# Optimization experiments

Measured on AMD Instinct MI355X. Metric: run time of the kernel, lower is better.

## Reference

```python
import jax, jax.numpy as jnp
import numpy as np
import math

B, T, D, H = 8, 1024, 512, 8
DK = D // H


def setup_inputs() -> dict:
    key = jax.random.key(0)
    ks = jax.random.split(key, 16)
    f = lambda k, s: jax.random.normal(k, s, dtype=jnp.float32)
    p = lambda k, s: jax.random.normal(k, s, dtype=jnp.float32) * 0.02
    return {
        "query": f(ks[0], (B, T, D)),
        "key": f(ks[1], (B, T, D)),
        "value": f(ks[2], (B, T, D)),
        "pos_embedding": f(ks[3], (B, T, D)),
        "Wq": p(ks[4], (D, D)), "bq": p(ks[5], (D,)),
        "Wk": p(ks[6], (D, D)), "bk": p(ks[7], (D,)),
        "Wv": p(ks[8], (D, D)), "bv": p(ks[9], (D,)),
        "Wp": p(ks[10], (D, D)),
        "u_bias": p(ks[11], (H, DK)),
        "v_bias": p(ks[12], (H, DK)),
        "Wo": p(ks[13], (D, D)), "bo": p(ks[14], (D,)),
    }


def _rel_shift(pos_score):
    # pos_score: [B, H, T, T]  -> Transformer-XL relative shift via pad/reshape
    b, h, t1, t2 = pos_score.shape
    padded = jnp.concatenate(
        [jnp.zeros((b, h, t1, 1), pos_score.dtype), pos_score], axis=-1
    )  # [B,H,T,T+1]
    padded = padded.reshape(b, h, t2 + 1, t1)
    return padded[:, :, 1:].reshape(b, h, t1, t2)


def reference(query, key, value, pos_embedding, Wq, bq, Wk, bk, Wv, bv, Wp,
              u_bias, v_bias, Wo, bo):
    q = (query @ Wq + bq).reshape(B, T, H, DK)          # [B,T,H,DK]
    k = (key @ Wk + bk).reshape(B, T, H, DK)
    v = (value @ Wv + bv).reshape(B, T, H, DK)
    p = (pos_embedding @ Wp).reshape(B, T, H, DK)

    content_score = jnp.einsum("bihd,bjhd->bhij", q + u_bias, k)
    pos_score = jnp.einsum("bihd,bjhd->bhij", q + v_bias, p)
    pos_score = _rel_shift(pos_score)

    score = (content_score + pos_score) / math.sqrt(D)  # note: sqrt(d_model)
    attn = jax.nn.softmax(score, axis=-1)               # dropout: eval mode
    context = jnp.einsum("bhij,bjhd->bihd", attn, v).reshape(B, T, D)
    return context @ Wo + bo
```

## Files before the change

### kernel.cpp

```cpp
#include <hip/hip_runtime.h>

#define B_ 8
#define T_ 1024
#define D_ 512
#define H_ 8
#define DK_ 64

typedef __bf16 bf16x8 __attribute__((ext_vector_type(8)));
typedef float f32x4 __attribute__((ext_vector_type(4)));

#define MFMA16(a, b, c) __builtin_amdgcn_mfma_f32_16x16x32_bf16(a, b, c, 0, 0, 0)

__device__ __forceinline__ bf16x8 pack8(float4 a, float4 b) {
  bf16x8 r;
  r[0] = (__bf16)a.x; r[1] = (__bf16)a.y; r[2] = (__bf16)a.z; r[3] = (__bf16)a.w;
  r[4] = (__bf16)b.x; r[5] = (__bf16)b.y; r[6] = (__bf16)b.z; r[7] = (__bf16)b.w;
  return r;
}

__device__ __forceinline__ void load_lds16(const void* g, void* l) {
  __builtin_amdgcn_global_load_lds(
      (const __attribute__((address_space(1))) void*)g,
      (__attribute__((address_space(3))) void*)l, 16, 0, 0);
}

__global__ __launch_bounds__(256) void cvt_w(const float* __restrict__ w0,
                                             const float* __restrict__ w1,
                                             const float* __restrict__ w2,
                                             const float* __restrict__ w3,
                                             const float* __restrict__ w4,
                                             __bf16* __restrict__ wt) {
  __shared__ float Ts[64][65];
  const float* W = (blockIdx.z == 0) ? w0
                 : (blockIdx.z == 1) ? w1
                 : (blockIdx.z == 2) ? w2
                 : (blockIdx.z == 3) ? w3 : w4;
  const int tid = threadIdx.x;
  const int kt = blockIdx.x * 64, nt = blockIdx.y * 64;
  const int r = tid >> 2, co = (tid & 3) * 16;
#pragma unroll
  for (int q = 0; q < 4; ++q)
    *(float4*)&Ts[r][co + q * 4] =
        *(const float4*)(W + (size_t)(kt + r) * 512 + nt + co + q * 4);
  __syncthreads();
  bf16x8 o0, o1;
#pragma unroll
  for (int q = 0; q < 8; ++q) o0[q] = (__bf16)Ts[co + q][r];
#pragma unroll
  for (int q = 0; q < 8; ++q) o1[q] = (__bf16)Ts[co + 8 + q][r];
  const int key = r & 7;
  __bf16* dst =
      wt + (size_t)blockIdx.z * 262144 + (size_t)(nt + r) * 512 + kt;
  *(bf16x8*)(dst + (((co >> 3) ^ key) << 3)) = o0;
  *(bf16x8*)(dst + ((((co >> 3) + 1) ^ key) << 3)) = o1;
}

__global__ __launch_bounds__(256, 4) void gemm_dma(
    const float* __restrict__ qf, const float* __restrict__ kf,
    const float* __restrict__ vf, const float* __restrict__ pf,
    const __bf16* __restrict__ Wt, const float* __restrict__ bq,
    const float* __restrict__ bk, const float* __restrict__ bv,
    const float* __restrict__ ub, const float* __restrict__ vb,
    __bf16* __restrict__ quB, __bf16* __restrict__ qvB,
    __bf16* __restrict__ kB, __bf16* __restrict__ vT,
    __bf16* __restrict__ pB) {
  __shared__ __bf16 smem[17408];
  __bf16* As = smem;
  __bf16* Bs = smem + 8192;
  const int tid = threadIdx.x;
  const int z = blockIdx.z;
  const int wave = tid >> 6, lane = tid & 63, l16 = lane & 15, quad = lane >> 4;
  const int wm = wave & 1, wn = wave >> 1;
  const int m0 = blockIdx.x * 128, n0 = blockIdx.y * 128;

  const float* Af = (z == 0) ? qf : (z == 1) ? kf : (z == 2) ? vf : pf;
  const __bf16* Bg = Wt + (size_t)z * (512 * 512);

  const int drow = tid >> 3, dch = (tid & 7) * 8;
  char* ldsB = (char*)Bs + (tid & 192) * 16;
  const int keyc = l16 & 7;

  f32x4 acc[4][4];
#pragma unroll
  for (int rb = 0; rb < 4; ++rb)
#pragma unroll
    for (int cb = 0; cb < 4; ++cb) acc[rb][cb] = 0.f;

#pragma unroll 1
  for (int k0 = 0; k0 < 512; k0 += 64) {
    __syncthreads();
#pragma unroll
    for (int c4 = 0; c4 < 4; ++c4)
      load_lds16(Bg + (size_t)(n0 + c4 * 32 + drow) * 512 + k0 + dch,
                 ldsB + c4 * 4096);
#pragma unroll
    for (int c4 = 0; c4 < 4; ++c4) {
      const int row = c4 * 32 + drow;
      const float* s = Af + (size_t)(m0 + row) * 512 + k0 + dch;
      float4 a0 = *(const float4*)s;
      float4 a1 = *(const float4*)(s + 4);
      *(bf16x8*)&As[row * 64 + ((((dch >> 3) ^ row) & 7) << 3)] =
          pack8(a0, a1);
    }
    __syncthreads();
#pragma unroll
    for (int s = 0; s < 2; ++s) {
      const int ph = ((s * 4 + quad) ^ keyc) << 3;
      bf16x8 afr[4], bfr[4];
#pragma unroll
      for (int rb = 0; rb < 4; ++rb)
        afr[rb] = *(const bf16x8*)&As[(wm * 64 + rb * 16 + l16) * 64 + ph];
#pragma unroll
      for (int cb = 0; cb < 4; ++cb)
        bfr[cb] = *(const bf16x8*)&Bs[(wn * 64 + cb * 16 + l16) * 64 + ph];
#pragma unroll
      for (int rb = 0; rb < 4; ++rb)
#pragma unroll
        for (int cb = 0; cb < 4; ++cb)
          acc[rb][cb] = MFMA16(afr[rb], bfr[cb], acc[rb][cb]);
    }
  }

  __syncthreads();

  if (z == 2) {
    __bf16* Tt = smem;
#pragma unroll
    for (int rb = 0; rb < 4; ++rb)
#pragma unroll
      for (int cb = 0; cb < 4; ++cb) {
        const int cl = wn * 64 + cb * 16 + l16;
        const float bb = bv[n0 + cl];
#pragma unroll
        for (int r = 0; r < 4; ++r) {
          const int rl = wm * 64 + rb * 16 + quad * 4 + r;
          Tt[cl * 136 + rl] = (__bf16)(acc[rb][cb][r] + bb);
        }
      }
    __syncthreads();
    const int r2 = tid >> 1, ch = (tid & 1) * 64;
    const int hh = (n0 + r2) >> 6, dkk = (n0 + r2) & 63;
    const int bI = m0 >> 10, t0 = m0 & 1023;
    __bf16* dst = vT + (((size_t)(bI * H_ + hh)) * DK_ + dkk) * T_ + t0 + ch;
    const int vkey = dkk & 7;
#pragma unroll
    for (int q = 0; q < 8; ++q)
      *(bf16x8*)(dst + ((q ^ vkey) * 8)) =
          *(const bf16x8*)&Tt[r2 * 136 + ch + q * 8];
    return;
  }

  __bf16* Tt = smem;
  const int trow = tid & 127, hs = tid >> 7;
  const int bI = m0 >> 10, tt = (m0 & 1023) + trow;
  const int hh = (n0 >> 6) + hs;
  const size_t obase = (((size_t)(bI * H_ + hh)) * T_ + tt) * DK_;
  const int npass = (z == 0) ? 2 : 1;
#pragma unroll 1
  for (int pass = 0; pass < npass; ++pass) {
#pragma unroll
    for (int rb = 0; rb < 4; ++rb)
#pragma unroll
      for (int cb = 0; cb < 4; ++cb) {
        const int cl = wn * 64 + cb * 16 + l16;
        const int col = n0 + cl;
        const float b0 = (z == 0) ? bq[col] : (z == 1) ? bk[col] : 0.f;
        const float b1 = (z == 0) ? (pass ? vb[col] : ub[col]) : 0.f;
#pragma unroll
        for (int r = 0; r < 4; ++r) {
          const int rl = wm * 64 + rb * 16 + quad * 4 + r;
          Tt[rl * 136 + cl] = (__bf16)((acc[rb][cb][r] + b0) + b1);
        }
      }
    __syncthreads();
    __bf16* dst = ((z == 0) ? (pass ? qvB : quB) : (z == 1) ? kB : pB) + obase;
#pragma unroll
    for (int qd = 0; qd < 8; ++qd) {
      const int c = (z == 0) ? qd : (qd ^ (tt & 7));
      *(bf16x8*)(dst + c * 8) =
          *(const bf16x8*)&Tt[trow * 136 + hs * 64 + qd * 8];
    }
    if (pass + 1 < npass) __syncthreads();
  }
}

__global__ __launch_bounds__(256, 4) void gemm_out(
    const __bf16* __restrict__ ctxA, const __bf16* __restrict__ Wo,
    const float* __restrict__ bo, float* __restrict__ out) {
  __shared__ __bf16 As[4096];
  __shared__ __bf16 Bs[8192];
  const int tid = threadIdx.x;
  const int wave = tid >> 6, lane = tid & 63, l16 = lane & 15, quad = lane >> 4;
  const int m0 = blockIdx.x * 64, n0 = blockIdx.y * 128;

  const int drow = tid >> 3, dch = (tid & 7) * 8;
  char* ldsA = (char*)As + (tid & 192) * 16;
  char* ldsB = (char*)Bs + (tid & 192) * 16;
  const int keyc = l16 & 7;

  f32x4 acc[4][2];
#pragma unroll
  for (int rb = 0; rb < 4; ++rb)
#pragma unroll
    for (int cb = 0; cb < 2; ++cb) acc[rb][cb] = 0.f;

#pragma unroll 1
  for (int k0 = 0; k0 < 512; k0 += 64) {
    __syncthreads();
#pragma unroll
    for (int c4 = 0; c4 < 2; ++c4)
      load_lds16(ctxA + (size_t)(m0 + c4 * 32 + drow) * 512 + k0 + dch,
                 ldsA + c4 * 4096);
#pragma unroll
    for (int c4 = 0; c4 < 4; ++c4)
      load_lds16(Wo + (size_t)(n0 + c4 * 32 + drow) * 512 + k0 + dch,
                 ldsB + c4 * 4096);
    __syncthreads();
#pragma unroll
    for (int s = 0; s < 2; ++s) {
      const int ph = ((s * 4 + quad) ^ keyc) << 3;
      bf16x8 afr[4], bfr[2];
#pragma unroll
      for (int rb = 0; rb < 4; ++rb)
        afr[rb] = *(const bf16x8*)&As[(rb * 16 + l16) * 64 + ph];
#pragma unroll
      for (int cb = 0; cb < 2; ++cb)
        bfr[cb] = *(const bf16x8*)&Bs[(wave * 32 + cb * 16 + l16) * 64 + ph];
#pragma unroll
      for (int rb = 0; rb < 4; ++rb)
#pragma unroll
        for (int cb = 0; cb < 2; ++cb)
          acc[rb][cb] = MFMA16(afr[rb], bfr[cb], acc[rb][cb]);
    }
  }

#pragma unroll
  for (int rb = 0; rb < 4; ++rb)
#pragma unroll
    for (int cb = 0; cb < 2; ++cb) {
      const int col = n0 + wave * 32 + cb * 16 + l16;
      const float bb = bo[col];
#pragma unroll
      for (int r = 0; r < 4; ++r) {
        const int row = m0 + rb * 16 + quad * 4 + r;
        out[(size_t)row * 512 + col] = acc[rb][cb][r] + bb;
      }
    }
}

__global__ __launch_bounds__(256, 4) void attn_mfma(
    const __bf16* __restrict__ qu, const __bf16* __restrict__ qv,
    const __bf16* __restrict__ kbuf, const __bf16* __restrict__ vT,
    const __bf16* __restrict__ pbuf, __bf16* __restrict__ ctx) {
  constexpr float SCALE2 = 0.06375871865f;
  __shared__ __bf16 smemA[4488];
  __shared__ __bf16 Vt[4096];
  __shared__ __bf16 Pb[8192];
  __bf16* Kt = smemA;
  __bf16* Rs = smemA;
  __bf16* Pa = Pb;

  const int tid = threadIdx.x;
  const int wave = tid >> 6, lane = tid & 63, l16 = lane & 15, quad = lane >> 4;
  const int g = blockIdx.x;
  const int bhq = (g & 7) * 8 + (g >> 7);
  const int i0 = ((g >> 3) & 15) * 64;
  const size_t bh = (size_t)bhq * T_ * DK_;
  const __bf16* QU = qu + bh;
  const __bf16* QV = qv + bh;
  const __bf16* Kg = kbuf + bh;
  const __bf16* Vg = vT + bh;
  const __bf16* Pg = pbuf + bh;

  bf16x8 quA[2], qvw[2], qv4[2];
  {
    const int rw = i0 + wave * 16 + l16;
    const int r4g = i0 + 64 + l16;
    const int r4 = (r4g < T_) ? r4g : T_ - 1;
#pragma unroll
    for (int s = 0; s < 2; ++s) {
      const int ko = s * 32 + quad * 8;
      quA[s] = *(const bf16x8*)&QU[(size_t)rw * DK_ + ko];
      qvw[s] = *(const bf16x8*)&QV[(size_t)rw * DK_ + ko];
      qv4[s] = *(const bf16x8*)&QV[(size_t)r4 * DK_ + ko];
    }
  }

  f32x4 Oacc[4];
#pragma unroll
  for (int cb = 0; cb < 4; ++cb) Oacc[cb] = 0.f;
  float lrun[4];
#pragma unroll
  for (int r = 0; r < 4; ++r) lrun[r] = 0.f;

  const int rbase = wave * 16 + quad * 4;
  const int keyr = l16 & 7;
  const int keyp = (l16 + 7) & 7;
  const int drow = tid >> 3;
  const int dch = (tid & 7) * 8;
  char* ldsK = (char*)Kt + (tid & 192) * 16;
  char* ldsV = (char*)Vt + (tid & 192) * 16;
  char* ldsP = (char*)Pb + (tid & 192) * 16;

#pragma unroll 1
  for (int jt = 0; jt < 16; ++jt) {
    const int j0 = jt * 64;
    int cs = T_ - 65 + j0 - i0;
    if (cs < 0) cs += T_;
    if (cs >= T_) cs -= T_;

    __syncthreads();
    load_lds16(Kg + (size_t)(j0 + drow) * 64 + dch, ldsK);
    load_lds16(Kg + (size_t)(j0 + 32 + drow) * 64 + dch, ldsK + 4096);
    __builtin_amdgcn_sched_barrier(0);
    load_lds16(Vg + (size_t)drow * T_ + j0 + dch, ldsV);
    load_lds16(Vg + (size_t)(32 + drow) * T_ + j0 + dch, ldsV + 4096);
#pragma unroll
    for (int c = 0; c < 4; ++c) {
      int prow = cs + c * 32 + drow;
      if (prow >= T_) prow -= T_;
      load_lds16(Pg + (size_t)prow * 64 + dch, ldsP + c * 4096);
    }
    asm volatile("s_waitcnt vmcnt(6)" ::: "memory");
    __builtin_amdgcn_s_barrier();

    f32x4 sA[4];
#pragma unroll
    for (int cb = 0; cb < 4; ++cb) sA[cb] = 0.f;
    __builtin_amdgcn_s_setprio(1);
#pragma unroll
    for (int s = 0; s < 2; ++s)
#pragma unroll
      for (int cb = 0; cb < 4; ++cb) {
        bf16x8 kf = *(const bf16x8*)&Kt[(cb * 16 + l16) * 64 +
                                        (((s * 4 + quad) ^ keyr) << 3)];
        sA[cb] = MFMA16(quA[s], kf, sA[cb]);
      }
    __builtin_amdgcn_s_setprio(0);

    asm volatile("s_waitcnt vmcnt(0)" ::: "memory");
    __builtin_amdgcn_s_barrier();

    __builtin_amdgcn_s_setprio(1);
#pragma unroll
    for (int c = 0; c < 5; ++c) {
      const int cb = 3 - wave + c;
      f32x4 rc = 0.f;
#pragma unroll
      for (int s = 0; s < 2; ++s) {
        bf16x8 pf = *(const bf16x8*)&Pb[(cb * 16 + l16) * 64 +
                                        (((s * 4 + quad) ^ keyp) << 3)];
        rc = MFMA16(qvw[s], pf, rc);
      }
      const int col = cb * 16 + l16;
#pragma unroll
      for (int rr = 0; rr < 4; ++rr) {
        const int dj = col + rbase + rr - 64;
        if (dj >= 0 && dj < 64) Rs[(rbase + rr) * 68 + dj] = (__bf16)rc[rr];
      }
    }
    {
      const int cb = wave;
      f32x4 rc = 0.f;
#pragma unroll
      for (int s = 0; s < 2; ++s) {
        bf16x8 pf = *(const bf16x8*)&Pb[(cb * 16 + l16) * 64 +
                                        (((s * 4 + quad) ^ keyp) << 3)];
        rc = MFMA16(qv4[s], pf, rc);
      }
      if (quad == 0) Rs[64 * 68 + cb * 16 + l16] = (__bf16)rc[0];
    }
    __builtin_amdgcn_s_setprio(0);
    __syncthreads();

    const int delta = j0 - i0;
    if (delta == 0 || delta == 64) {
#pragma unroll
      for (int r = 0; r < 4; ++r) {
#pragma unroll
        for (int cb = 0; cb < 4; ++cb) {
          const int di = rbase + r;
          const int dj = cb * 16 + l16;
          const int ji = delta + dj - di;
          float pos = 0.f;
          if (ji != 1) pos = (float)Rs[(di + (ji >= 2 ? 1 : 0)) * 68 + dj];
          const float w_ = exp2f((sA[cb][r] + pos) * SCALE2);
          lrun[r] += w_;
          Pa[di * 64 + (dj & 7) + ((((dj >> 3) ^ di) & 7) << 3)] = (__bf16)w_;
        }
      }
    } else {
      const int cadd = (delta >= 128) ? 1 : 0;
#pragma unroll
      for (int r = 0; r < 4; ++r) {
#pragma unroll
        for (int cb = 0; cb < 4; ++cb) {
          const int di = rbase + r;
          const int dj = cb * 16 + l16;
          const float pos = (float)Rs[(di + cadd) * 68 + dj];
          const float w_ = exp2f((sA[cb][r] + pos) * SCALE2);
          lrun[r] += w_;
          Pa[di * 64 + (dj & 7) + ((((dj >> 3) ^ di) & 7) << 3)] = (__bf16)w_;
        }
      }
    }

    __builtin_amdgcn_s_setprio(1);
#pragma unroll
    for (int s = 0; s < 2; ++s) {
      bf16x8 ap = *(const bf16x8*)&Pa[(wave * 16 + l16) * 64 +
                                      (((s * 4 + quad) ^ keyr) << 3)];
#pragma unroll
      for (int cb = 0; cb < 4; ++cb) {
        bf16x8 bv = *(const bf16x8*)&Vt[(cb * 16 + l16) * 64 +
                                        (((s * 4 + quad) ^ keyr) << 3)];
        Oacc[cb] = MFMA16(ap, bv, Oacc[cb]);
      }
    }
    __builtin_amdgcn_s_setprio(0);
  }

  float inv[4];
#pragma unroll
  for (int r = 0; r < 4; ++r) {
    float L = lrun[r];
    L += __shfl_xor(L, 1);
    L += __shfl_xor(L, 2);
    L += __shfl_xor(L, 4);
    L += __shfl_xor(L, 8);
    inv[r] = 1.f / L;
  }
  const int b = bhq >> 3, h = bhq & 7;
#pragma unroll
  for (int cb = 0; cb < 4; ++cb)
#pragma unroll
    for (int r = 0; r < 4; ++r) {
      const int row = i0 + rbase + r;
      const int chunk = cb * 2 + (l16 >> 3);
      const int col = h * DK_ + ((chunk ^ (row & 7)) << 3) + (l16 & 7);
      ctx[((size_t)(b * T_ + row)) * D_ + col] = (__bf16)(Oacc[cb][r] * inv[r]);
    }
}

extern "C" void kernel_launch(void* const* d_in, const int* in_sizes, int n_in,
                              void* d_out, int out_size, void* d_ws,
                              size_t ws_size, hipStream_t stream) {
  const float* query = (const float*)d_in[0];
  const float* key   = (const float*)d_in[1];
  const float* value = (const float*)d_in[2];
  const float* pos   = (const float*)d_in[3];
  const float* Wq = (const float*)d_in[4];
  const float* bq = (const float*)d_in[5];
  const float* Wk = (const float*)d_in[6];
  const float* bk = (const float*)d_in[7];
  const float* Wv = (const float*)d_in[8];
  const float* bv = (const float*)d_in[9];
  const float* Wp = (const float*)d_in[10];
  const float* ub = (const float*)d_in[11];
  const float* vbias = (const float*)d_in[12];
  const float* Wo = (const float*)d_in[13];
  const float* bo = (const float*)d_in[14];
  float* out = (float*)d_out;

  char* ws = (char*)d_ws;
  const size_t ACT = (size_t)8192 * 512 * 2;
  __bf16* quB = (__bf16*)ws;
  __bf16* qvB = (__bf16*)(ws + 1 * ACT);
  __bf16* kB  = (__bf16*)(ws + 2 * ACT);
  __bf16* pB  = (__bf16*)(ws + 3 * ACT);
  __bf16* vT  = (__bf16*)(ws + 4 * ACT);
  __bf16* ctx = (__bf16*)(ws + 5 * ACT);
  __bf16* Wt  = (__bf16*)(ws + 6 * ACT);

  cvt_w<<<dim3(8, 8, 5), 256, 0, stream>>>(Wq, Wk, Wv, Wp, Wo, Wt);

  gemm_dma<<<dim3(64, 4, 4), 256, 0, stream>>>(
      query, key, value, pos, Wt, bq, bk, bv, ub, vbias,
      quB, qvB, kB, vT, pB);

  attn_mfma<<<dim3(1024), 256, 0, stream>>>(quB, qvB, kB, vT, pB, ctx);

  gemm_out<<<dim3(128, 4), 256, 0, stream>>>(ctx, Wt + 4 * 262144, bo, out);
}
```

Before: 244.9 us.

## Software-pipeline projection and output GEMMs with register prefetch and double-buffered LDS

In the QKVP projection GEMM, the next K-tile of fp32 activations is prefetched into registers while the current tile computes. As is double-buffered in LDS, and explicit s_barrier/s_waitcnt replace __syncthreads. The output GEMM double-buffers both A and B tiles, so the next tile's global-to-LDS DMA is issued before computing the current one. The aim is to hide global load latency behind MFMA work, at the cost of more LDS and registers, which lowers the occupancy hints to 3 and 2.

```diff
diff --git a/kernel.cpp b/kernel.cpp
--- a/kernel.cpp
+++ b/kernel.cpp
@@ -55,7 +55,7 @@
   *(bf16x8*)(dst + ((((co >> 3) + 1) ^ key) << 3)) = o1;
 }
 
-__global__ __launch_bounds__(256, 4) void gemm_dma(
+__global__ __launch_bounds__(256, 3) void gemm_dma(
     const float* __restrict__ qf, const float* __restrict__ kf,
     const float* __restrict__ vf, const float* __restrict__ pf,
     const __bf16* __restrict__ Wt, const float* __restrict__ bq,
@@ -64,9 +64,9 @@
     __bf16* __restrict__ quB, __bf16* __restrict__ qvB,
     __bf16* __restrict__ kB, __bf16* __restrict__ vT,
     __bf16* __restrict__ pB) {
-  __shared__ __bf16 smem[17408];
+  __shared__ __bf16 smem[24576];
   __bf16* As = smem;
-  __bf16* Bs = smem + 8192;
+  __bf16* Bs = smem + 16384;
   const int tid = threadIdx.x;
   const int z = blockIdx.z;
   const int wave = tid >> 6, lane = tid & 63, l16 = lane & 15, quad = lane >> 4;
@@ -79,37 +79,61 @@
   const int drow = tid >> 3, dch = (tid & 7) * 8;
   char* ldsB = (char*)Bs + (tid & 192) * 16;
   const int keyc = l16 & 7;
+  const int arow_sw = ((((dch >> 3)) & 7) << 3);
 
   f32x4 acc[4][4];
 #pragma unroll
   for (int rb = 0; rb < 4; ++rb)
 #pragma unroll
     for (int cb = 0; cb < 4; ++cb) acc[rb][cb] = 0.f;
+
+  float4 pa[4][2];
+#pragma unroll
+  for (int c4 = 0; c4 < 4; ++c4) {
+    const float* s = Af + (size_t)(m0 + c4 * 32 + drow) * 512 + dch;
+    pa[c4][0] = *(const float4*)s;
+    pa[c4][1] = *(const float4*)(s + 4);
+  }
 
 #pragma unroll 1
   for (int k0 = 0; k0 < 512; k0 += 64) {
-    __syncthreads();
+    const int cur = (k0 >> 6) & 1;
+    __builtin_amdgcn_s_barrier();
+
+#pragma unroll
+    for (int c4 = 0; c4 < 4; ++c4) {
+      const int row = c4 * 32 + drow;
+      *(bf16x8*)&As[cur * 8192 + row * 64 + ((((dch >> 3) ^ row) & 7) << 3)] =
+          pack8(pa[c4][0], pa[c4][1]);
+    }
+    __builtin_amdgcn_sched_barrier(0);
 #pragma unroll
     for (int c4 = 0; c4 < 4; ++c4)
       load_lds16(Bg + (size_t)(n0 + c4 * 32 + drow) * 512 + k0 + dch,
                  ldsB + c4 * 4096);
-#pragma unroll
-    for (int c4 = 0; c4 < 4; ++c4) {
-      const int row = c4 * 32 + drow;
-      const float* s = Af + (size_t)(m0 + row) * 512 + k0 + dch;
-      float4 a0 = *(const float4*)s;
-      float4 a1 = *(const float4*)(s + 4);
-      *(bf16x8*)&As[row * 64 + ((((dch >> 3) ^ row) & 7) << 3)] =
-          pack8(a0, a1);
-    }
-    __syncthreads();
+    __builtin_amdgcn_sched_barrier(0);
+    if (k0 + 64 < 512) {
+#pragma unroll
+      for (int c4 = 0; c4 < 4; ++c4) {
+        const float* s = Af + (size_t)(m0 + c4 * 32 + drow) * 512 + k0 + 64 + dch;
+        pa[c4][0] = *(const float4*)s;
+        pa[c4][1] = *(const float4*)(s + 4);
+      }
+      __builtin_amdgcn_sched_barrier(0);
+      asm volatile("s_waitcnt vmcnt(4) lgkmcnt(0)" ::: "memory");
+    } else {
+      asm volatile("s_waitcnt vmcnt(0) lgkmcnt(0)" ::: "memory");
+    }
+    __builtin_amdgcn_s_barrier();
+
 #pragma unroll
     for (int s = 0; s < 2; ++s) {
       const int ph = ((s * 4 + quad) ^ keyc) << 3;
       bf16x8 afr[4], bfr[4];
 #pragma unroll
       for (int rb = 0; rb < 4; ++rb)
-        afr[rb] = *(const bf16x8*)&As[(wm * 64 + rb * 16 + l16) * 64 + ph];
+        afr[rb] = *(const bf16x8*)&As[cur * 8192 +
+                                      (wm * 64 + rb * 16 + l16) * 64 + ph];
 #pragma unroll
       for (int cb = 0; cb < 4; ++cb)
         bfr[cb] = *(const bf16x8*)&Bs[(wn * 64 + cb * 16 + l16) * 64 + ph];
@@ -184,11 +208,11 @@
   }
 }
 
-__global__ __launch_bounds__(256, 4) void gemm_out(
+__global__ __launch_bounds__(256, 2) void gemm_out(
     const __bf16* __restrict__ ctxA, const __bf16* __restrict__ Wo,
     const float* __restrict__ bo, float* __restrict__ out) {
-  __shared__ __bf16 As[4096];
-  __shared__ __bf16 Bs[8192];
+  __shared__ __bf16 As[2][4096];
+  __shared__ __bf16 Bs[2][8192];
   const int tid = threadIdx.x;
   const int wave = tid >> 6, lane = tid & 63, l16 = lane & 15, quad = lane >> 4;
   const int m0 = blockIdx.x * 64, n0 = blockIdx.y * 128;
@@ -204,28 +228,41 @@
 #pragma unroll
     for (int cb = 0; cb < 2; ++cb) acc[rb][cb] = 0.f;
 
+#define GO_ISSUE(KK, BUF)                                                     \
+  {                                                                           \
+    _Pragma("unroll") for (int c4 = 0; c4 < 2; ++c4)                          \
+        load_lds16(ctxA + (size_t)(m0 + c4 * 32 + drow) * 512 + (KK) + dch,   \
+                   ldsA + (BUF) * 8192 + c4 * 4096);                          \
+    _Pragma("unroll") for (int c4 = 0; c4 < 4; ++c4)                          \
+        load_lds16(Wo + (size_t)(n0 + c4 * 32 + drow) * 512 + (KK) + dch,     \
+                   ldsB + (BUF) * 16384 + c4 * 4096);                         \
+  }
+
+  GO_ISSUE(0, 0)
+
 #pragma unroll 1
   for (int k0 = 0; k0 < 512; k0 += 64) {
-    __syncthreads();
-#pragma unroll
-    for (int c4 = 0; c4 < 2; ++c4)
-      load_lds16(ctxA + (size_t)(m0 + c4 * 32 + drow) * 512 + k0 + dch,
-                 ldsA + c4 * 4096);
-#pragma unroll
-    for (int c4 = 0; c4 < 4; ++c4)
-      load_lds16(Wo + (size_t)(n0 + c4 * 32 + drow) * 512 + k0 + dch,
-                 ldsB + c4 * 4096);
-    __syncthreads();
+    const int cur = (k0 >> 6) & 1;
+    __builtin_amdgcn_s_barrier();
+    if (k0 + 64 < 512) {
+      GO_ISSUE(k0 + 64, cur ^ 1)
+      __builtin_amdgcn_sched_barrier(0);
+      asm volatile("s_waitcnt vmcnt(6)" ::: "memory");
+    } else {
+      asm volatile("s_waitcnt vmcnt(0)" ::: "memory");
+    }
+    __builtin_amdgcn_s_barrier();
+
 #pragma unroll
     for (int s = 0; s < 2; ++s) {
       const int ph = ((s * 4 + quad) ^ keyc) << 3;
       bf16x8 afr[4], bfr[2];
 #pragma unroll
       for (int rb = 0; rb < 4; ++rb)
-        afr[rb] = *(const bf16x8*)&As[(rb * 16 + l16) * 64 + ph];
+        afr[rb] = *(const bf16x8*)&As[cur][(rb * 16 + l16) * 64 + ph];
 #pragma unroll
       for (int cb = 0; cb < 2; ++cb)
-        bfr[cb] = *(const bf16x8*)&Bs[(wave * 32 + cb * 16 + l16) * 64 + ph];
+        bfr[cb] = *(const bf16x8*)&Bs[cur][(wave * 32 + cb * 16 + l16) * 64 + ph];
 #pragma unroll
       for (int rb = 0; rb < 4; ++rb)
 #pragma unroll
```

Result: no change. 243.5 us (-0.6%).
